# Kernel optimization log

Hardware: AMD Instinct MI355X
Metric: run time of the kernel (lower is better)

## Reference

```python
import jax, jax.numpy as jnp
import numpy as np
from jax import lax

B, N = 16, 4096


def _fps(xyz, npoint):
    # xyz: [N,3] -> [npoint] int32 indices (iterative farthest point sampling, start at idx 0)
    n = xyz.shape[0]
    def step(carry, _):
        dist, far = carry
        d = jnp.sum((xyz - xyz[far]) ** 2, axis=-1)
        dist = jnp.minimum(dist, d)
        nxt = jnp.argmax(dist).astype(jnp.int32)
        return (dist, nxt), far
    (_, _), idx = lax.scan(step, (jnp.full((n,), 1e10, xyz.dtype), jnp.int32(0)), None, length=npoint)
    return idx


def _ball_query(xyz, new_xyz, radius, nsample):
    # xyz: [N,3], new_xyz: [S,3] -> [S, nsample] neighbor indices within radius
    n = xyz.shape[0]
    sqr = jnp.sum((new_xyz[:, None, :] - xyz[None, :, :]) ** 2, axis=-1)  # [S,N]
    idx = jnp.where(sqr > radius * radius, n, jnp.arange(n)[None, :])
    idx = jnp.sort(idx, axis=-1)[:, :nsample]
    return jnp.where(idx == n, idx[:, :1], idx)  # pad misses with first hit


def _gather(p, i):
    return p[i]


def _mlp(feat, ws):
    # feat: [B,S,K,C]; 1x1 conv + folded eval-BN + ReLU per layer
    for W, b in ws:
        feat = jax.nn.relu(jnp.einsum('bskc,oc->bsko', feat, W) + b)
    return feat


def _sa(xyz, points, npoint, radius, nsample, ws):
    fps_idx = jax.vmap(_fps, in_axes=(0, None))(xyz, npoint)              # [B,S]
    new_xyz = jnp.take_along_axis(xyz, fps_idx[..., None], axis=1)         # [B,S,3]
    idx = jax.vmap(_ball_query, in_axes=(0, 0, None, None))(xyz, new_xyz, radius, nsample)  # [B,S,K]
    grouped_xyz = jax.vmap(_gather)(xyz, idx) - new_xyz[:, :, None, :]     # [B,S,K,3]
    if points is None:
        feat = grouped_xyz
    else:
        feat = jnp.concatenate([grouped_xyz, jax.vmap(_gather)(points, idx)], axis=-1)
    return new_xyz, jnp.max(_mlp(feat, ws), axis=2)                        # [B,S,Cout]


def _forward(x, ws1, ws2, ws3, fw, fb):
    b = x.shape[0]
    l1_xyz, l1_pts = _sa(x, None, 512, 0.2, 32, ws1)       # [B,512,3], [B,512,128]
    l2_xyz, l2_pts = _sa(l1_xyz, l1_pts, 128, 0.4, 64, ws2)  # [B,128,3], [B,128,256]
    feat = jnp.concatenate([l2_xyz, l2_pts], axis=-1)[:, None]  # group_all: [B,1,128,259]
    g = jnp.max(_mlp(feat, ws3), axis=2).reshape(b, 1024)
    return g @ fw.T + fb


_SPECS = [
    ('sa1_w0', (64, 3)), ('sa1_b0', (64,)), ('sa1_w1', (64, 64)), ('sa1_b1', (64,)), ('sa1_w2', (128, 64)), ('sa1_b2', (128,)),
    ('sa2_w0', (128, 131)), ('sa2_b0', (128,)), ('sa2_w1', (128, 128)), ('sa2_b1', (128,)), ('sa2_w2', (256, 128)), ('sa2_b2', (256,)),
    ('sa3_w0', (256, 259)), ('sa3_b0', (256,)), ('sa3_w1', (512, 256)), ('sa3_b1', (512,)), ('sa3_w2', (1024, 512)), ('sa3_b2', (1024,)),
    ('fw', (1024, 1024)), ('fb', (1024,)),
]


def setup_inputs() -> dict:
    key = jax.random.key(0)
    keys = jax.random.split(key, len(_SPECS) + 1)
    inp = {'x': jax.random.uniform(keys[0], (B, N, 3), dtype=jnp.float32)}
    for (name, shp), k in zip(_SPECS, keys[1:]):
        inp[name] = jax.random.normal(k, shp, dtype=jnp.float32) * 0.02
    return inp


def reference(x, sa1_w0, sa1_b0, sa1_w1, sa1_b1, sa1_w2, sa1_b2,
              sa2_w0, sa2_b0, sa2_w1, sa2_b1, sa2_w2, sa2_b2,
              sa3_w0, sa3_b0, sa3_w1, sa3_b1, sa3_w2, sa3_b2, fw, fb):
    ws1 = [(sa1_w0, sa1_b0), (sa1_w1, sa1_b1), (sa1_w2, sa1_b2)]
    ws2 = [(sa2_w0, sa2_b0), (sa2_w1, sa2_b1), (sa2_w2, sa2_b2)]
    ws3 = [(sa3_w0, sa3_b0), (sa3_w1, sa3_b1), (sa3_w2, sa3_b2)]
    return _forward(x, ws1, ws2, ws3, fw, fb)
```

## Files before the change

### kernel.cpp

```cpp
#include <hip/hip_runtime.h>

#ifndef BATCH
#define BATCH 16
#endif

typedef float f32x2 __attribute__((ext_vector_type(2)));
__device__ __forceinline__ f32x2 mk2(float a, float b) { f32x2 r; r.x = a; r.y = b; return r; }

template<int CTRL>
__device__ __forceinline__ float dppmaxf(float v)
{
    const int d = __builtin_amdgcn_update_dpp(__float_as_int(v), __float_as_int(v),
                                              CTRL, 0xf, 0xf, false);
    return fmaxf(v, __int_as_float(d));
}
template<int CTRL>
__device__ __forceinline__ unsigned dppminu(unsigned v)
{
    const unsigned d = (unsigned)__builtin_amdgcn_update_dpp((int)v, (int)v,
                                                             CTRL, 0xf, 0xf, false);
    return (d < v) ? d : v;
}
__device__ __forceinline__ float wave_max_bcast(float v)
{
    v = dppmaxf<0x111>(v);
    v = dppmaxf<0x112>(v);
    v = dppmaxf<0x114>(v);
    v = dppmaxf<0x118>(v);
    v = dppmaxf<0x142>(v);
    v = dppmaxf<0x143>(v);
    return __int_as_float(__builtin_amdgcn_readlane(__float_as_int(v), 63));
}
__device__ __forceinline__ unsigned wave_min_bcast(unsigned v)
{
    v = dppminu<0x111>(v);
    v = dppminu<0x112>(v);
    v = dppminu<0x114>(v);
    v = dppminu<0x118>(v);
    v = dppminu<0x142>(v);
    v = dppminu<0x143>(v);
    return (unsigned)__builtin_amdgcn_readlane((int)v, 63);
}

template<int N, int NP1, int NP2, int BLOCK>
__global__ __launch_bounds__(BLOCK)
void fps_fused(const float* __restrict__ xyz,
               float* __restrict__ out1, float* __restrict__ out2)
{
#pragma clang fp contract(off)
    constexpr int P  = N / BLOCK;
    constexpr int P2 = NP1 / BLOCK;
    constexpr int NW = BLOCK / 64;
    __shared__ float sx[N], sy[N], sz[N];
    __shared__ float s2x[NP1], s2y[NP1], s2z[NP1];
    __shared__ float o2x[NP2], o2y[NP2], o2z[NP2];
    __shared__ unsigned long long wslot[2][NW];
    const int b = blockIdx.x, t = threadIdx.x;
    const int lane = t & 63, wv = t >> 6;
    const float* xb = xyz + (size_t)b * N * 3;
    float px[P], py[P], pz[P], dist[P];
#pragma unroll
    for (int j = 0; j < P; ++j) {
        const int i = t + j * BLOCK;
        const float x = xb[i*3+0], y = xb[i*3+1], z = xb[i*3+2];
        sx[i] = x; sy[i] = y; sz[i] = z;
        px[j] = x; py[j] = y; pz[j] = z;
        dist[j] = 1e10f;
    }
    __syncthreads();
    float fx = sx[0], fy = sy[0], fz = sz[0];
    if (t == 0) { s2x[0] = fx; s2y[0] = fy; s2z[0] = fz; }
    for (int s = 1; s < NP1; ++s) {
        float bestv = -1.f; int besti = 0;
#pragma unroll
        for (int j = 0; j < P; ++j) {
            const float dx = px[j]-fx, dy = py[j]-fy, dz = pz[j]-fz;
            const float d = (dx*dx + dy*dy) + dz*dz;
            const float nd = fminf(dist[j], d);
            dist[j] = nd;
            if (nd > bestv) { bestv = nd; besti = t + j * BLOCK; }
        }
        const float wm = wave_max_bcast(bestv);
        const unsigned cand = (bestv == wm) ? (unsigned)besti : 0xffffffffu;
        const unsigned wi = wave_min_bcast(cand);
        const int par = s & 1;
        if (lane == 0)
            wslot[par][wv] = ((unsigned long long)__float_as_uint(wm) << 32)
                           | (unsigned)(~wi);
        __syncthreads();
        unsigned long long pa = wslot[par][0];
#pragma unroll
        for (int w = 1; w < NW; ++w) {
            const unsigned long long pb = wslot[par][w];
            pa = (pb > pa) ? pb : pa;
        }
        const int far = (int)(~(unsigned)pa);
        fx = sx[far]; fy = sy[far]; fz = sz[far];
        if (t == 0) { s2x[s] = fx; s2y[s] = fy; s2z[s] = fz; }
    }
    __syncthreads();
    float mx[P2], my[P2], mz[P2], d2[P2];
#pragma unroll
    for (int j = 0; j < P2; ++j) {
        const int i = t + j * BLOCK;
        mx[j] = s2x[i]; my[j] = s2y[i]; mz[j] = s2z[i];
        d2[j] = 1e10f;
    }
    fx = s2x[0]; fy = s2y[0]; fz = s2z[0];
    if (t == 0) { o2x[0] = fx; o2y[0] = fy; o2z[0] = fz; }
    for (int s = 1; s < NP2; ++s) {
        float bestv = -1.f; int besti = 0;
#pragma unroll
        for (int j = 0; j < P2; ++j) {
            const float dx = mx[j]-fx, dy = my[j]-fy, dz = mz[j]-fz;
            const float d = (dx*dx + dy*dy) + dz*dz;
            const float nd = fminf(d2[j], d);
            d2[j] = nd;
            if (nd > bestv) { bestv = nd; besti = t + j * BLOCK; }
        }
        const float wm = wave_max_bcast(bestv);
        const unsigned cand = (bestv == wm) ? (unsigned)besti : 0xffffffffu;
        const unsigned wi = wave_min_bcast(cand);
        const int par = s & 1;
        if (lane == 0)
            wslot[par][wv] = ((unsigned long long)__float_as_uint(wm) << 32)
                           | (unsigned)(~wi);
        __syncthreads();
        unsigned long long pa = wslot[par][0];
#pragma unroll
        for (int w = 1; w < NW; ++w) {
            const unsigned long long pb = wslot[par][w];
            pa = (pb > pa) ? pb : pa;
        }
        const int far2 = (int)(~(unsigned)pa);
        fx = s2x[far2]; fy = s2y[far2]; fz = s2z[far2];
        if (t == 0) { o2x[s] = fx; o2y[s] = fy; o2z[s] = fz; }
    }
    __syncthreads();
    for (int i = t; i < NP1; i += BLOCK) {
        out1[((size_t)b*NP1 + i)*3 + 0] = s2x[i];
        out1[((size_t)b*NP1 + i)*3 + 1] = s2y[i];
        out1[((size_t)b*NP1 + i)*3 + 2] = s2z[i];
    }
    for (int i = t; i < NP2; i += BLOCK) {
        out2[((size_t)b*NP2 + i)*3 + 0] = o2x[i];
        out2[((size_t)b*NP2 + i)*3 + 1] = o2y[i];
        out2[((size_t)b*NP2 + i)*3 + 2] = o2z[i];
    }
}

template<int N, int S, int K>
__device__ __forceinline__ void ballq_body(const float* __restrict__ xyz,
                                           const float* __restrict__ nxyz,
                                           int* __restrict__ idx, const float r2,
                                           const int bid, const int tid)
{
#pragma clang fp contract(off)
    const int gw = (bid * 256 + tid) >> 6;
    const int lane = tid & 63;
    const int b = gw / S, s = gw % S;
    const float* xb = xyz + (size_t)b * N * 3;
    const float qx = nxyz[((size_t)b*S + s)*3 + 0];
    const float qy = nxyz[((size_t)b*S + s)*3 + 1];
    const float qz = nxyz[((size_t)b*S + s)*3 + 2];
    int* op = idx + ((size_t)b*S + s) * K;
    int base = 0, first = -1;
    for (int c = 0; c < N; c += 64) {
        const int i = c + lane;
        const float dx = xb[i*3+0]-qx, dy = xb[i*3+1]-qy, dz = xb[i*3+2]-qz;
        const float d = (dx*dx + dy*dy) + dz*dz;
        const bool hit = !(d > r2);
        const unsigned long long m = __ballot(hit);
        if (first < 0 && m) first = c + __builtin_ctzll(m);
        const int pos = base + __popcll(m & ((1ull << lane) - 1ull));
        if (hit && pos < K) op[pos] = i;
        base += __popcll(m);
        if (base >= K) break;
    }
    if (base < K && lane >= base && lane < K) op[lane] = first;
}

__global__ __launch_bounds__(256)
void ballq_both(const float* __restrict__ pts1, const float* __restrict__ q1,
                int* __restrict__ idx1, const float r2a,
                const float* __restrict__ pts2, const float* __restrict__ q2,
                int* __restrict__ idx2, const float r2b)
{
    const int nb1 = (BATCH * 512) / 4;
    if ((int)blockIdx.x < nb1)
        ballq_body<4096, 512, 32>(pts1, q1, idx1, r2a, blockIdx.x, threadIdx.x);
    else
        ballq_body<512, 128, 64>(pts2, q2, idx2, r2b, blockIdx.x - nb1, threadIdx.x);
}

__global__ __launch_bounds__(256)
void transpose_all(const float* __restrict__ s0, float* __restrict__ d0,
                   const float* __restrict__ s1, float* __restrict__ d1,
                   const float* __restrict__ s2, float* __restrict__ d2,
                   const float* __restrict__ s3, float* __restrict__ d3,
                   const float* __restrict__ s4, float* __restrict__ d4,
                   const float* __restrict__ s5, float* __restrict__ d5,
                   const float* __restrict__ s6, float* __restrict__ d6,
                   const float* __restrict__ s7, float* __restrict__ d7,
                   const float* __restrict__ s8, float* __restrict__ d8)
{
    int i = blockIdx.x * 256 + threadIdx.x;
    if (i < 192)    { d0[(i%3)  *64   + i/3  ] = s0[i]; return; }  i -= 192;
    if (i < 4096)   { d1[(i&63) *64   + (i>>6)] = s1[i]; return; } i -= 4096;
    if (i < 8192)   { d2[(i&63) *128  + (i>>6)] = s2[i]; return; } i -= 8192;
    if (i < 16768)  { d3[(i%131)*128  + i/131] = s3[i]; return; }  i -= 16768;
    if (i < 16384)  { d4[(i&127)*128  + (i>>7)] = s4[i]; return; } i -= 16384;
    if (i < 32768)  { d5[(i&127)*256  + (i>>7)] = s5[i]; return; } i -= 32768;
    if (i < 66304)  { d6[(i%259)*256  + i/259] = s6[i]; return; }  i -= 66304;
    if (i < 131072) { d7[(i&255)*512  + (i>>8)] = s7[i]; return; } i -= 131072;
    if (i < 524288) { d8[(i&511)*1024 + (i>>9)] = s8[i]; return; }
}

__device__ __forceinline__ void fma16pk(f32x2 (&acc)[8], const float f,
                                        const float* __restrict__ wrow)
{
    const float4 w0 = ((const float4*)wrow)[0];
    const float4 w1 = ((const float4*)wrow)[1];
    const float4 w2 = ((const float4*)wrow)[2];
    const float4 w3 = ((const float4*)wrow)[3];
    const f32x2 ff = mk2(f, f);
    acc[0] += ff * mk2(w0.x, w0.y);
    acc[1] += ff * mk2(w0.z, w0.w);
    acc[2] += ff * mk2(w1.x, w1.y);
    acc[3] += ff * mk2(w1.z, w1.w);
    acc[4] += ff * mk2(w2.x, w2.y);
    acc[5] += ff * mk2(w2.z, w2.w);
    acc[6] += ff * mk2(w3.x, w3.y);
    acc[7] += ff * mk2(w3.z, w3.w);
}

__device__ __forceinline__ float pool_half(float v)
{
    v = fmaxf(v, __shfl_xor(v, 1));
    v = fmaxf(v, __shfl_xor(v, 2));
    v = fmaxf(v, __shfl_xor(v, 4));
    v = fmaxf(v, __shfl_xor(v, 8));
    v = fmaxf(v, __shfl_xor(v, 16));
    return v;
}
__device__ __forceinline__ float pool_full(float v)
{
    v = pool_half(v);
    return fmaxf(v, __shfl_xor(v, 32));
}

__global__ __launch_bounds__(256)
void sa1_fused(const float* __restrict__ xyz, const float* __restrict__ nxyz,
               const int* __restrict__ idx,
               const float* __restrict__ Wt0, const float* __restrict__ B0,
               const float* __restrict__ Wt1, const float* __restrict__ B1,
               const float* __restrict__ Wt2, const float* __restrict__ B2,
               float* __restrict__ out)
{
    __shared__ float buf[64][64];
    const int tid = threadIdx.x, lane = tid & 63;
    const int wave = __builtin_amdgcn_readfirstlane(tid >> 6);
    const int row0 = blockIdx.x * 64;
    const int myrow = row0 + lane;
    const int g = myrow >> 5, b = g >> 9;
    const int i = idx[myrow];
    const float* p = xyz + ((size_t)b*4096 + i) * 3;
    const float f0 = p[0] - nxyz[(size_t)g*3 + 0];
    const float f1 = p[1] - nxyz[(size_t)g*3 + 1];
    const float f2 = p[2] - nxyz[(size_t)g*3 + 2];
    const int oc0 = wave * 16;
    f32x2 aL[8], aH[8];
#pragma unroll
    for (int j = 0; j < 16; ++j) {
        const float v = B0[oc0+j] + f0*Wt0[0*64+oc0+j] + f1*Wt0[1*64+oc0+j] + f2*Wt0[2*64+oc0+j];
        buf[oc0+j][lane] = fmaxf(v, 0.f);
    }
    __syncthreads();
#pragma unroll
    for (int k = 0; k < 8; ++k) aL[k] = mk2(B1[oc0+2*k], B1[oc0+2*k+1]);
#pragma unroll 4
    for (int ci = 0; ci < 64; ++ci)
        fma16pk(aL, buf[ci][lane], Wt1 + ci*64 + oc0);
    __syncthreads();
#pragma unroll
    for (int k = 0; k < 8; ++k) {
        buf[oc0+2*k][lane]   = fmaxf(aL[k].x, 0.f);
        buf[oc0+2*k+1][lane] = fmaxf(aL[k].y, 0.f);
    }
    __syncthreads();
#pragma unroll
    for (int k = 0; k < 8; ++k) {
        aL[k] = mk2(B2[oc0+2*k], B2[oc0+2*k+1]);
        aH[k] = mk2(B2[64+oc0+2*k], B2[64+oc0+2*k+1]);
    }
#pragma unroll 2
    for (int ci = 0; ci < 64; ++ci) {
        const float f = buf[ci][lane];
        fma16pk(aL, f, Wt2 + ci*128 + oc0);
        fma16pk(aH, f, Wt2 + ci*128 + 64 + oc0);
    }
#pragma unroll
    for (int k = 0; k < 8; ++k) {
        const float v0 = pool_half(fmaxf(aL[k].x, 0.f));
        const float v1 = pool_half(fmaxf(aL[k].y, 0.f));
        const float w0 = pool_half(fmaxf(aH[k].x, 0.f));
        const float w1 = pool_half(fmaxf(aH[k].y, 0.f));
        if ((lane & 31) == 0) {
            const size_t orow = (size_t)((row0 + lane) >> 5) * 128;
            out[orow + oc0 + 2*k]       = v0;
            out[orow + oc0 + 2*k + 1]   = v1;
            out[orow + 64 + oc0 + 2*k]     = w0;
            out[orow + 64 + oc0 + 2*k + 1] = w1;
        }
    }
}

__global__ __launch_bounds__(256)
void sa2_fused(const float* __restrict__ l1xyz, const float* __restrict__ l1pts,
               const float* __restrict__ nxyz, const int* __restrict__ idx,
               const float* __restrict__ Wt0, const float* __restrict__ B0,
               const float* __restrict__ Wt1, const float* __restrict__ B1,
               const float* __restrict__ Wt2, const float* __restrict__ B2,
               float* __restrict__ out)
{
    __shared__ float buf[128][64];
    const int tid = threadIdx.x, lane = tid & 63;
    const int wave = __builtin_amdgcn_readfirstlane(tid >> 6);
    const int gblk = blockIdx.x;
    const int b = gblk >> 7;
    const int row0 = gblk * 64;
    const int myi = idx[row0 + lane];
    const float* pc = l1xyz + ((size_t)b*512 + myi) * 3;
    const float f0 = pc[0] - nxyz[(size_t)gblk*3 + 0];
    const float f1 = pc[1] - nxyz[(size_t)gblk*3 + 1];
    const float f2 = pc[2] - nxyz[(size_t)gblk*3 + 2];
    for (int r = wave; r < 64; r += 4) {
        const int i2 = idx[row0 + r];
        const float* src = l1pts + ((size_t)b*512 + i2) * 128;
        buf[lane][r ^ lane]    = src[lane];
        buf[lane+64][r ^ lane] = src[lane + 64];
    }
    __syncthreads();
    const int oc0 = wave * 16;
    f32x2 aL[8], aH[8];
#pragma unroll
    for (int k = 0; k < 8; ++k) {
        const int j0 = oc0 + 2*k, j1 = oc0 + 2*k + 1;
        aL[k] = mk2(B0[j0]    + f0*Wt0[j0]     + f1*Wt0[128+j0]    + f2*Wt0[256+j0],
                    B0[j1]    + f0*Wt0[j1]     + f1*Wt0[128+j1]    + f2*Wt0[256+j1]);
        aH[k] = mk2(B0[64+j0] + f0*Wt0[64+j0]  + f1*Wt0[192+j0]    + f2*Wt0[320+j0],
                    B0[64+j1] + f0*Wt0[64+j1]  + f1*Wt0[192+j1]    + f2*Wt0[320+j1]);
    }
#pragma unroll 2
    for (int ci = 0; ci < 128; ++ci) {
        const float f = buf[ci][lane ^ (ci & 63)];
        const float* wp = Wt0 + (size_t)(ci+3)*128;
        fma16pk(aL, f, wp + oc0);
        fma16pk(aH, f, wp + 64 + oc0);
    }
    __syncthreads();
#pragma unroll
    for (int k = 0; k < 8; ++k) {
        buf[oc0+2*k][lane]      = fmaxf(aL[k].x, 0.f);
        buf[oc0+2*k+1][lane]    = fmaxf(aL[k].y, 0.f);
        buf[64+oc0+2*k][lane]   = fmaxf(aH[k].x, 0.f);
        buf[64+oc0+2*k+1][lane] = fmaxf(aH[k].y, 0.f);
    }
    __syncthreads();
#pragma unroll
    for (int k = 0; k < 8; ++k) {
        aL[k] = mk2(B1[oc0+2*k], B1[oc0+2*k+1]);
        aH[k] = mk2(B1[64+oc0+2*k], B1[64+oc0+2*k+1]);
    }
#pragma unroll 2
    for (int ci = 0; ci < 128; ++ci) {
        const float f = buf[ci][lane];
        const float* wp = Wt1 + (size_t)ci*128;
        fma16pk(aL, f, wp + oc0);
        fma16pk(aH, f, wp + 64 + oc0);
    }
    __syncthreads();
#pragma unroll
    for (int k = 0; k < 8; ++k) {
        buf[oc0+2*k][lane]      = fmaxf(aL[k].x, 0.f);
        buf[oc0+2*k+1][lane]    = fmaxf(aL[k].y, 0.f);
        buf[64+oc0+2*k][lane]   = fmaxf(aH[k].x, 0.f);
        buf[64+oc0+2*k+1][lane] = fmaxf(aH[k].y, 0.f);
    }
    __syncthreads();
    float* orow = out + (size_t)gblk * 256;
    for (int half = 0; half < 2; ++half) {
        const int oc = half*128 + oc0;
#pragma unroll
        for (int k = 0; k < 8; ++k) {
            aL[k] = mk2(B2[oc+2*k], B2[oc+2*k+1]);
            aH[k] = mk2(B2[64+oc+2*k], B2[64+oc+2*k+1]);
        }
#pragma unroll 2
        for (int ci = 0; ci < 128; ++ci) {
            const float f = buf[ci][lane];
            const float* wp = Wt2 + (size_t)ci*256;
            fma16pk(aL, f, wp + oc);
            fma16pk(aH, f, wp + 64 + oc);
        }
#pragma unroll
        for (int k = 0; k < 8; ++k) {
            const float v0 = pool_full(fmaxf(aL[k].x, 0.f));
            const float v1 = pool_full(fmaxf(aL[k].y, 0.f));
            const float w0 = pool_full(fmaxf(aH[k].x, 0.f));
            const float w1 = pool_full(fmaxf(aH[k].y, 0.f));
            if (lane == 0) {
                orow[oc + 2*k]        = v0;
                orow[oc + 2*k + 1]    = v1;
                orow[64 + oc + 2*k]   = w0;
                orow[64 + oc + 2*k+1] = w1;
            }
        }
    }
}

template<int CIN, int COUT, bool CONCAT3, bool POOL>
__global__ __launch_bounds__(256)
void mlp_gemm_kernel(const float* __restrict__ inA, const float* __restrict__ inB,
                     const float* __restrict__ Wt, const float* __restrict__ Bb,
                     float* __restrict__ out)
{
    __shared__ float featS[128][64];
    const int tid = threadIdx.x, lane = tid & 63;
    const int wave = __builtin_amdgcn_readfirstlane(tid >> 6);
    const int row0 = blockIdx.x * 64;
    const int oc0 = blockIdx.y * 64 + wave * 16;
    f32x2 acc[8];
#pragma unroll
    for (int k = 0; k < 8; ++k) acc[k] = mk2(Bb[oc0+2*k], Bb[oc0+2*k+1]);
    for (int c0 = 0; c0 < CIN; c0 += 128) {
        const int csz = (CIN - c0 < 128) ? (CIN - c0) : 128;
        __syncthreads();
        for (int r = wave; r < 64; r += 4) {
            const int row = row0 + r;
            for (int cl = lane; cl < csz; cl += 64) {
                const int cig = c0 + cl;
                float v;
                if (CONCAT3)
                    v = (cig < 3) ? inA[(size_t)row*3 + cig]
                                  : inB[(size_t)row*(CIN-3) + (cig - 3)];
                else
                    v = inA[(size_t)row*CIN + cig];
                featS[cl][r ^ (cl & 63)] = v;
            }
        }
        __syncthreads();
        if (csz == 128) {
#pragma unroll 4
            for (int ci = 0; ci < 128; ++ci)
                fma16pk(acc, featS[ci][lane ^ (ci & 63)], Wt + (size_t)(c0+ci)*COUT + oc0);
        } else {
            for (int ci = 0; ci < csz; ++ci)
                fma16pk(acc, featS[ci][lane ^ (ci & 63)], Wt + (size_t)(c0+ci)*COUT + oc0);
        }
    }
    if (POOL) {
#pragma unroll
        for (int k = 0; k < 8; ++k) {
            const float v0 = pool_full(fmaxf(acc[k].x, 0.f));
            const float v1 = pool_full(fmaxf(acc[k].y, 0.f));
            if (lane == 0) {
                out[(size_t)blockIdx.x * COUT + oc0 + 2*k]     = v0;
                out[(size_t)blockIdx.x * COUT + oc0 + 2*k + 1] = v1;
            }
        }
    } else {
        float4 o0, o1, o2, o3;
        o0.x=fmaxf(acc[0].x,0.f); o0.y=fmaxf(acc[0].y,0.f); o0.z=fmaxf(acc[1].x,0.f); o0.w=fmaxf(acc[1].y,0.f);
        o1.x=fmaxf(acc[2].x,0.f); o1.y=fmaxf(acc[2].y,0.f); o1.z=fmaxf(acc[3].x,0.f); o1.w=fmaxf(acc[3].y,0.f);
        o2.x=fmaxf(acc[4].x,0.f); o2.y=fmaxf(acc[4].y,0.f); o2.z=fmaxf(acc[5].x,0.f); o2.w=fmaxf(acc[5].y,0.f);
        o3.x=fmaxf(acc[6].x,0.f); o3.y=fmaxf(acc[6].y,0.f); o3.z=fmaxf(acc[7].x,0.f); o3.w=fmaxf(acc[7].y,0.f);
        float4* op = (float4*)(out + (size_t)(row0 + lane)*COUT + oc0);
        op[0]=o0; op[1]=o1; op[2]=o2; op[3]=o3;
    }
}

__global__ __launch_bounds__(256)
void fc_kernel(const float* __restrict__ pmax, const float* __restrict__ fw,
               const float* __restrict__ fb, float* __restrict__ y)
{
    const int gw = (blockIdx.x * 256 + threadIdx.x) >> 6;
    const int lane = threadIdx.x & 63;
    const int b = gw >> 10, o = gw & 1023;
    const float4* g0 = (const float4*)(pmax + (size_t)(2*b) * 1024);
    const float4* g1 = (const float4*)(pmax + (size_t)(2*b+1) * 1024);
    const float4* wv = (const float4*)(fw + (size_t)o * 1024);
    float acc = 0.f;
#pragma unroll
    for (int r = 0; r < 4; ++r) {
        const float4 a = g0[lane + r*64];
        const float4 c = g1[lane + r*64];
        const float4 w = wv[lane + r*64];
        acc += fmaxf(a.x,c.x)*w.x + fmaxf(a.y,c.y)*w.y
             + fmaxf(a.z,c.z)*w.z + fmaxf(a.w,c.w)*w.w;
    }
#pragma unroll
    for (int m = 32; m >= 1; m >>= 1) acc += __shfl_xor(acc, m);
    if (lane == 0) y[gw] = acc + fb[o];
}

extern "C" void kernel_launch(void* const* d_in, const int* in_sizes, int n_in,
                              void* d_out, int out_size, void* d_ws, size_t ws_size,
                              hipStream_t stream)
{
    (void)in_sizes; (void)n_in; (void)out_size; (void)ws_size;
    const float* x   = (const float*)d_in[0];
    const float* s1w0 = (const float*)d_in[1];  const float* s1b0 = (const float*)d_in[2];
    const float* s1w1 = (const float*)d_in[3];  const float* s1b1 = (const float*)d_in[4];
    const float* s1w2 = (const float*)d_in[5];  const float* s1b2 = (const float*)d_in[6];
    const float* s2w0 = (const float*)d_in[7];  const float* s2b0 = (const float*)d_in[8];
    const float* s2w1 = (const float*)d_in[9];  const float* s2b1 = (const float*)d_in[10];
    const float* s2w2 = (const float*)d_in[11]; const float* s2b2 = (const float*)d_in[12];
    const float* s3w0 = (const float*)d_in[13]; const float* s3b0 = (const float*)d_in[14];
    const float* s3w1 = (const float*)d_in[15]; const float* s3b1 = (const float*)d_in[16];
    const float* s3w2 = (const float*)d_in[17]; const float* s3b2 = (const float*)d_in[18];
    const float* fw  = (const float*)d_in[19]; const float* fb  = (const float*)d_in[20];
    float* y = (float*)d_out;

    char* ws = (char*)d_ws;
    float* l1_xyz = (float*)(ws + 0);
    int*   idx1   = (int*)  (ws + 98304);
    float* l1_pts = (float*)(ws + 1146880);
    float* l2_xyz = (float*)(ws + 5341184);
    int*   idx2   = (int*)  (ws + 5365760);
    float* l2_pts = (float*)(ws + 5890048);
    float* h1     = (float*)(ws + 7987200);
    float* h2     = (float*)(ws + 10084352);
    float* pmax   = (float*)(ws + 14278656);
    float* wt1_0  = (float*)(ws + 14409728);
    float* wt1_1  = (float*)(ws + 14410496);
    float* wt1_2  = (float*)(ws + 14426880);
    float* wt2_0  = (float*)(ws + 14459648);
    float* wt2_1  = (float*)(ws + 14526720);
    float* wt2_2  = (float*)(ws + 14592256);
    float* wt3_0  = (float*)(ws + 14723328);
    float* wt3_1  = (float*)(ws + 14988544);
    float* wt3_2  = (float*)(ws + 15512832);

    const float r2_1 = (float)(0.2 * 0.2);
    const float r2_2 = (float)(0.4 * 0.4);

    transpose_all<<<3126, 256, 0, stream>>>(
        s1w0, wt1_0, s1w1, wt1_1, s1w2, wt1_2,
        s2w0, wt2_0, s2w1, wt2_1, s2w2, wt2_2,
        s3w0, wt3_0, s3w1, wt3_1, s3w2, wt3_2);

    fps_fused<4096, 512, 128, 256><<<BATCH, 256, 0, stream>>>(x, l1_xyz, l2_xyz);
    ballq_both<<<(BATCH*512)/4 + (BATCH*128)/4, 256, 0, stream>>>(
        x, l1_xyz, idx1, r2_1, l1_xyz, l2_xyz, idx2, r2_2);
    sa1_fused<<<(BATCH*512*32)/64, 256, 0, stream>>>(x, l1_xyz, idx1,
        wt1_0, s1b0, wt1_1, s1b1, wt1_2, s1b2, l1_pts);
    sa2_fused<<<BATCH*128, 256, 0, stream>>>(l1_xyz, l1_pts, l2_xyz, idx2,
        wt2_0, s2b0, wt2_1, s2b1, wt2_2, s2b2, l2_pts);
    mlp_gemm_kernel<259, 256,  true,  false><<<dim3(32, 4),  256, 0, stream>>>(l2_xyz, l2_pts, wt3_0, s3b0, h1);
    mlp_gemm_kernel<256, 512,  false, false><<<dim3(32, 8),  256, 0, stream>>>(h1, nullptr, wt3_1, s3b1, h2);
    mlp_gemm_kernel<512, 1024, false, true ><<<dim3(32, 16), 256, 0, stream>>>(h2, nullptr, wt3_2, s3b2, pmax);
    fc_kernel<<<(BATCH*1024)/4, 256, 0, stream>>>(pmax, fw, fb, y);
}
```

Measured before the change: 939.5 us.

## Carry winner coordinates through FPS reduction and pack distance math into float2

The FPS kernel now keeps the farthest point's coordinates alongside its distance instead of an index. This removes the second wave-wide min reduction and the dependent shared-memory coordinate lookup on every iteration. Points are assigned contiguously per thread so that the distance updates can use packed two-wide float vectors. Ties are broken by lowest lane, then per-thread scan order, then lowest wave. Because each thread now owns a contiguous block of points, this may not pick the same index as the reference's argmax when distances are exactly equal.

```diff
diff --git a/kernel.cpp b/kernel.cpp
--- a/kernel.cpp
+++ b/kernel.cpp
@@ -13,13 +13,6 @@
     const int d = __builtin_amdgcn_update_dpp(__float_as_int(v), __float_as_int(v),
                                               CTRL, 0xf, 0xf, false);
     return fmaxf(v, __int_as_float(d));
-}
-template<int CTRL>
-__device__ __forceinline__ unsigned dppminu(unsigned v)
-{
-    const unsigned d = (unsigned)__builtin_amdgcn_update_dpp((int)v, (int)v,
-                                                             CTRL, 0xf, 0xf, false);
-    return (d < v) ? d : v;
 }
 __device__ __forceinline__ float wave_max_bcast(float v)
 {
@@ -31,16 +24,6 @@
     v = dppmaxf<0x143>(v);
     return __int_as_float(__builtin_amdgcn_readlane(__float_as_int(v), 63));
 }
-__device__ __forceinline__ unsigned wave_min_bcast(unsigned v)
-{
-    v = dppminu<0x111>(v);
-    v = dppminu<0x112>(v);
-    v = dppminu<0x114>(v);
-    v = dppminu<0x118>(v);
-    v = dppminu<0x142>(v);
-    v = dppminu<0x143>(v);
-    return (unsigned)__builtin_amdgcn_readlane((int)v, 63);
-}
 
 template<int N, int NP1, int NP2, int BLOCK>
 __global__ __launch_bounds__(BLOCK)
@@ -51,89 +34,106 @@
     constexpr int P  = N / BLOCK;
     constexpr int P2 = NP1 / BLOCK;
     constexpr int NW = BLOCK / 64;
-    __shared__ float sx[N], sy[N], sz[N];
     __shared__ float s2x[NP1], s2y[NP1], s2z[NP1];
     __shared__ float o2x[NP2], o2y[NP2], o2z[NP2];
-    __shared__ unsigned long long wslot[2][NW];
+    __shared__ unsigned long long wkey[2][NW];
+    __shared__ float wcx[2][NW], wcy[2][NW], wcz[2][NW];
     const int b = blockIdx.x, t = threadIdx.x;
     const int lane = t & 63, wv = t >> 6;
     const float* xb = xyz + (size_t)b * N * 3;
-    float px[P], py[P], pz[P], dist[P];
-#pragma unroll
-    for (int j = 0; j < P; ++j) {
-        const int i = t + j * BLOCK;
-        const float x = xb[i*3+0], y = xb[i*3+1], z = xb[i*3+2];
-        sx[i] = x; sy[i] = y; sz[i] = z;
-        px[j] = x; py[j] = y; pz[j] = z;
-        dist[j] = 1e10f;
-    }
-    __syncthreads();
-    float fx = sx[0], fy = sy[0], fz = sz[0];
+    f32x2 vpx[P/2], vpy[P/2], vpz[P/2], vdist[P/2];
+#pragma unroll
+    for (int k = 0; k < P/2; ++k) {
+        const int i = t*P + 2*k;
+        vpx[k] = mk2(xb[i*3+0], xb[i*3+3]);
+        vpy[k] = mk2(xb[i*3+1], xb[i*3+4]);
+        vpz[k] = mk2(xb[i*3+2], xb[i*3+5]);
+        vdist[k] = mk2(1e10f, 1e10f);
+    }
+    float fx = xb[0], fy = xb[1], fz = xb[2];
     if (t == 0) { s2x[0] = fx; s2y[0] = fy; s2z[0] = fz; }
+    __syncthreads();
     for (int s = 1; s < NP1; ++s) {
-        float bestv = -1.f; int besti = 0;
-#pragma unroll
-        for (int j = 0; j < P; ++j) {
-            const float dx = px[j]-fx, dy = py[j]-fy, dz = pz[j]-fz;
-            const float d = (dx*dx + dy*dy) + dz*dz;
-            const float nd = fminf(dist[j], d);
-            dist[j] = nd;
-            if (nd > bestv) { bestv = nd; besti = t + j * BLOCK; }
+        float bestv = -1.f, bx = 0.f, by = 0.f, bz = 0.f;
+        const f32x2 vfx = mk2(fx, fx), vfy = mk2(fy, fy), vfz = mk2(fz, fz);
+#pragma unroll
+        for (int k = 0; k < P/2; ++k) {
+            const f32x2 dx = vpx[k] - vfx;
+            const f32x2 dy = vpy[k] - vfy;
+            const f32x2 dz = vpz[k] - vfz;
+            const f32x2 d  = (dx*dx + dy*dy) + dz*dz;
+            const float nd0 = fminf(vdist[k].x, d.x);
+            const float nd1 = fminf(vdist[k].y, d.y);
+            vdist[k].x = nd0; vdist[k].y = nd1;
+            if (nd0 > bestv) { bestv = nd0; bx = vpx[k].x; by = vpy[k].x; bz = vpz[k].x; }
+            if (nd1 > bestv) { bestv = nd1; bx = vpx[k].y; by = vpy[k].y; bz = vpz[k].y; }
         }
         const float wm = wave_max_bcast(bestv);
-        const unsigned cand = (bestv == wm) ? (unsigned)besti : 0xffffffffu;
-        const unsigned wi = wave_min_bcast(cand);
+        const unsigned long long mask = __ballot(bestv == wm);
         const int par = s & 1;
-        if (lane == 0)
-            wslot[par][wv] = ((unsigned long long)__float_as_uint(wm) << 32)
-                           | (unsigned)(~wi);
+        if (lane == __builtin_ctzll(mask)) {
+            wkey[par][wv] = ((unsigned long long)__float_as_uint(wm) << 32)
+                          | (unsigned)(~wv);
+            wcx[par][wv] = bx; wcy[par][wv] = by; wcz[par][wv] = bz;
+        }
         __syncthreads();
-        unsigned long long pa = wslot[par][0];
+        unsigned long long ka = wkey[par][0];
+        float xa = wcx[par][0], ya = wcy[par][0], za = wcz[par][0];
 #pragma unroll
         for (int w = 1; w < NW; ++w) {
-            const unsigned long long pb = wslot[par][w];
-            pa = (pb > pa) ? pb : pa;
-        }
-        const int far = (int)(~(unsigned)pa);
-        fx = sx[far]; fy = sy[far]; fz = sz[far];
+            const unsigned long long kb = wkey[par][w];
+            const float xw = wcx[par][w], yw = wcy[par][w], zw = wcz[par][w];
+            if (kb > ka) { ka = kb; xa = xw; ya = yw; za = zw; }
+        }
+        fx = xa; fy = ya; fz = za;
         if (t == 0) { s2x[s] = fx; s2y[s] = fy; s2z[s] = fz; }
     }
     __syncthreads();
-    float mx[P2], my[P2], mz[P2], d2[P2];
-#pragma unroll
-    for (int j = 0; j < P2; ++j) {
-        const int i = t + j * BLOCK;
-        mx[j] = s2x[i]; my[j] = s2y[i]; mz[j] = s2z[i];
-        d2[j] = 1e10f;
+    f32x2 v2x[P2/2 > 0 ? P2/2 : 1], v2y[P2/2 > 0 ? P2/2 : 1],
+          v2z[P2/2 > 0 ? P2/2 : 1], v2d[P2/2 > 0 ? P2/2 : 1];
+#pragma unroll
+    for (int k = 0; k < P2/2; ++k) {
+        const int i = t*P2 + 2*k;
+        v2x[k] = mk2(s2x[i], s2x[i+1]);
+        v2y[k] = mk2(s2y[i], s2y[i+1]);
+        v2z[k] = mk2(s2z[i], s2z[i+1]);
+        v2d[k] = mk2(1e10f, 1e10f);
     }
     fx = s2x[0]; fy = s2y[0]; fz = s2z[0];
     if (t == 0) { o2x[0] = fx; o2y[0] = fy; o2z[0] = fz; }
     for (int s = 1; s < NP2; ++s) {
-        float bestv = -1.f; int besti = 0;
-#pragma unroll
-        for (int j = 0; j < P2; ++j) {
-            const float dx = mx[j]-fx, dy = my[j]-fy, dz = mz[j]-fz;
-            const float d = (dx*dx + dy*dy) + dz*dz;
-            const float nd = fminf(d2[j], d);
-            d2[j] = nd;
-            if (nd > bestv) { bestv = nd; besti = t + j * BLOCK; }
+        float bestv = -1.f, bx = 0.f, by = 0.f, bz = 0.f;
+        const f32x2 vfx = mk2(fx, fx), vfy = mk2(fy, fy), vfz = mk2(fz, fz);
+#pragma unroll
+        for (int k = 0; k < P2/2; ++k) {
+            const f32x2 dx = v2x[k] - vfx;
+            const f32x2 dy = v2y[k] - vfy;
+            const f32x2 dz = v2z[k] - vfz;
+            const f32x2 d  = (dx*dx + dy*dy) + dz*dz;
+            const float nd0 = fminf(v2d[k].x, d.x);
+            const float nd1 = fminf(v2d[k].y, d.y);
+            v2d[k].x = nd0; v2d[k].y = nd1;
+            if (nd0 > bestv) { bestv = nd0; bx = v2x[k].x; by = v2y[k].x; bz = v2z[k].x; }
+            if (nd1 > bestv) { bestv = nd1; bx = v2x[k].y; by = v2y[k].y; bz = v2z[k].y; }
         }
         const float wm = wave_max_bcast(bestv);
-        const unsigned cand = (bestv == wm) ? (unsigned)besti : 0xffffffffu;
-        const unsigned wi = wave_min_bcast(cand);
+        const unsigned long long mask = __ballot(bestv == wm);
         const int par = s & 1;
-        if (lane == 0)
-            wslot[par][wv] = ((unsigned long long)__float_as_uint(wm) << 32)
-                           | (unsigned)(~wi);
+        if (lane == __builtin_ctzll(mask)) {
+            wkey[par][wv] = ((unsigned long long)__float_as_uint(wm) << 32)
+                          | (unsigned)(~wv);
+            wcx[par][wv] = bx; wcy[par][wv] = by; wcz[par][wv] = bz;
+        }
         __syncthreads();
-        unsigned long long pa = wslot[par][0];
+        unsigned long long ka = wkey[par][0];
+        float xa = wcx[par][0], ya = wcy[par][0], za = wcz[par][0];
 #pragma unroll
         for (int w = 1; w < NW; ++w) {
-            const unsigned long long pb = wslot[par][w];
-            pa = (pb > pa) ? pb : pa;
-        }
-        const int far2 = (int)(~(unsigned)pa);
-        fx = s2x[far2]; fy = s2y[far2]; fz = s2z[far2];
+            const unsigned long long kb = wkey[par][w];
+            const float xw = wcx[par][w], yw = wcy[par][w], zw = wcz[par][w];
+            if (kb > ka) { ka = kb; xa = xw; ya = yw; za = zw; }
+        }
+        fx = xa; fy = ya; fz = za;
         if (t == 0) { o2x[s] = fx; o2y[s] = fy; o2z[s] = fz; }
     }
     __syncthreads();
```

New measurement: 1.019 ms. 8.4% more time.
